# Optimization experiments

Hardware: AMD Instinct MI355X
Metric: run time of the kernel (lower is better)

## Reference

```python
import jax, jax.numpy as jnp
import numpy as np

B, T, C = 4, 4096, 512
H, KS = 8, 9
D = C // H
PAD = KS // 2


def setup_inputs() -> dict:
    key = jax.random.key(0)
    ks = jax.random.split(key, 9)
    s = 1.0 / np.sqrt(C)
    return {
        "x": jax.random.normal(ks[0], (B, T, C), jnp.float32),
        "Wq": jax.random.normal(ks[1], (C, C), jnp.float32) * s,
        "bq": jax.random.normal(ks[2], (C,), jnp.float32) * 0.01,
        "Wk": jax.random.normal(ks[3], (C, C), jnp.float32) * s,
        "bk": jax.random.normal(ks[4], (C,), jnp.float32) * 0.01,
        "Wv": jax.random.normal(ks[5], (C, C), jnp.float32) * s,
        "bv": jax.random.normal(ks[6], (C,), jnp.float32) * 0.01,
        "Wo": jax.random.normal(ks[7], (C, C), jnp.float32) * s,
        "bo": jax.random.normal(ks[8], (C,), jnp.float32) * 0.01,
    }


def reference(x, Wq, bq, Wk, bk, Wv, bv, Wo, bo):
    Bx, Tx, Cx = x.shape
    # projections (torch Linear: x @ W.T + b), split heads -> (B,H,T,D)
    q = (x @ Wq.T + bq).reshape(Bx, Tx, H, D).transpose(0, 2, 1, 3)
    k = (x @ Wk.T + bk).reshape(Bx, Tx, H, D).transpose(0, 2, 1, 3)
    v = (x @ Wv.T + bv).reshape(Bx, Tx, H, D).transpose(0, 2, 1, 3)
    # replicate-pad along time (matches F.pad mode='replicate')
    k_pad = jnp.pad(k, ((0, 0), (0, 0), (PAD, PAD), (0, 0)), mode='edge')
    v_pad = jnp.pad(v, ((0, 0), (0, 0), (PAD, PAD), (0, 0)), mode='edge')
    # window gather indices: (T, KS) into padded time axis
    idx = jnp.arange(Tx)[:, None] + jnp.arange(KS)[None, :]
    k_unf = k_pad[:, :, idx, :]  # (B,H,T,KS,D)
    v_unf = v_pad[:, :, idx, :]  # (B,H,T,KS,D)
    scale = 1.0 / np.sqrt(D)
    scores = jnp.einsum('bhtd,bhtkd->bhtk', q, k_unf) * scale  # (B,H,T,KS)
    attn = jax.nn.softmax(scores, axis=-1)
    y = jnp.einsum('bhtk,bhtkd->bhtd', attn, v_unf)  # (B,H,T,D)
    y = y.transpose(0, 2, 1, 3).reshape(Bx, Tx, Cx)
    return y @ Wo.T + bo
```

## Files before the change

kernel.cpp:

```cpp
#include <hip/hip_runtime.h>
#include <hip/hip_bf16.h>

#define B_    4
#define T_    4096
#define C_    512
#define H_    8
#define D_    64
#define KS_   9
#define PAD_  4
#define MTOT  (B_ * T_)
#define PLANE (MTOT * C_)
#define WU    (C_ * C_ / 8)

typedef __bf16 bf16_t;
typedef __bf16 bf16x8 __attribute__((ext_vector_type(8)));
typedef float  f32x4  __attribute__((ext_vector_type(4)));

__global__ __launch_bounds__(256)
void conv_all(const float* __restrict__ Wq, const float* __restrict__ Wk,
              const float* __restrict__ Wv, const float* __restrict__ Wo,
              const float* __restrict__ x,
              bf16_t* __restrict__ Wb, bf16_t* __restrict__ xb) {
  int i = blockIdx.x * 256 + threadIdx.x;
  const float* src;
  bf16_t* dst;
  if (i < 4 * WU) {
    int w = i >> 15;
    const float* W = (w == 0) ? Wq : (w == 1) ? Wk : (w == 2) ? Wv : Wo;
    src = W + (size_t)(i & (WU - 1)) * 8;
    dst = Wb + (size_t)i * 8;
  } else {
    size_t j = (size_t)(i - 4 * WU);
    src = x + j * 8;
    dst = xb + j * 8;
  }
  float4 f0 = ((const float4*)src)[0];
  float4 f1 = ((const float4*)src)[1];
  bf16x8 o;
  o[0] = (bf16_t)f0.x; o[1] = (bf16_t)f0.y; o[2] = (bf16_t)f0.z; o[3] = (bf16_t)f0.w;
  o[4] = (bf16_t)f1.x; o[5] = (bf16_t)f1.y; o[6] = (bf16_t)f1.z; o[7] = (bf16_t)f1.w;
  *(bf16x8*)dst = o;
}

#define BM   256
#define BN   128
#define BK   64
#define NKT  (C_ / BK)
#define ASL  (BM * BK)
#define BSL  (BN * BK)
#define SLOT (ASL + BSL)

#define GLD(srcp, off) __builtin_amdgcn_global_load_lds(                     \
    (const __attribute__((address_space(1))) unsigned int*)(srcp),           \
    (__attribute__((address_space(3))) unsigned int*)(&sm[off]), 16, 0, 0)

template<int MODE>
__global__ __launch_bounds__(512, 2)
void gemm8p(const bf16_t* __restrict__ A, const bf16_t* __restrict__ Bw,
            const float* __restrict__ b0, const float* __restrict__ b1,
            const float* __restrict__ b2, void* __restrict__ Outp) {
  __shared__ __align__(16) bf16_t sm[3 * SLOT];

  constexpr int GX  = (MODE == 0) ? (3 * C_ / BN) : (C_ / BN);
  constexpr int NWG = GX * (MTOT / BM);
  constexpr int CPX = NWG / 8;

  const int ord = blockIdx.y * GX + blockIdx.x;
  const int lg  = (ord & 7) * CPX + (ord >> 3);
  const int n0  = (lg % GX) * BN;
  const int m0  = (lg / GX) * BM;

  const int tid  = threadIdx.x;
  const int lane = tid & 63;
  const int wave = tid >> 6;
  const int wm   = wave >> 2;
  const int wn   = wave & 3;

  const bf16_t* aSrc[4];
  const bf16_t* bSrc[2];
#pragma unroll
  for (int s = 0; s < 4; ++s) {
    int u = s * 512 + tid, r = u >> 3, ch = u & 7;
    int cs = (ch ^ (r & 7)) << 3;
    if (MODE == 0) {
      aSrc[s] = A + (size_t)(m0 + r) * C_ + cs;
    } else {
      int bb = m0 >> 12, t0 = m0 & (T_ - 1);
      aSrc[s] = A + ((size_t)bb * H_ * T_ + t0 + r) * D_ + cs;
    }
  }
#pragma unroll
  for (int s = 0; s < 2; ++s) {
    int u = s * 512 + tid, r = u >> 3, ch = u & 7;
    int cs = (ch ^ (r & 7)) << 3;
    bSrc[s] = Bw + (size_t)(n0 + r) * C_ + cs;
  }
  constexpr size_t ASTEP = (MODE == 0) ? (size_t)BK : (size_t)T_ * D_;

#pragma unroll
  for (int s = 0; s < 4; ++s) GLD(aSrc[s], (s * 512 + tid) * 8);
#pragma unroll
  for (int s = 0; s < 2; ++s) GLD(bSrc[s], ASL + (s * 512 + tid) * 8);
#pragma unroll
  for (int s = 0; s < 4; ++s) GLD(aSrc[s] + ASTEP, SLOT + (s * 512 + tid) * 8);
#pragma unroll
  for (int s = 0; s < 2; ++s) GLD(bSrc[s] + BK, SLOT + ASL + (s * 512 + tid) * 8);
  asm volatile("s_waitcnt vmcnt(6)" ::: "memory");
  __builtin_amdgcn_s_barrier();

  f32x4 acc[8][2] = {};
  const int lr  = lane & 15;
  const int lq  = lane >> 4;
  const int co0 = ((0 + lq) ^ (lane & 7)) << 3;
  const int co1 = ((4 + lq) ^ (lane & 7)) << 3;

  int rsl = 0;
  for (int kt = 0; kt < NKT; ++kt) {
    const bf16_t* arow = &sm[rsl * SLOT + (wm * 128 + lr) * 64];
    const bf16_t* brow = &sm[rsl * SLOT + ASL + (wn * 32 + lr) * 64];
    const int  wof = ((rsl == 0) ? 2 : rsl - 1) * SLOT;
    const bool st  = (kt + 2 < NKT);
    const size_t ka = (size_t)(kt + 2) * ASTEP;
    const size_t kb = (size_t)(kt + 2) * BK;

    bf16x8 af[4][2], bfr[2][2];

#pragma unroll
    for (int i = 0; i < 4; ++i) {
      af[i][0] = *(const bf16x8*)(arow + i * 1024 + co0);
      af[i][1] = *(const bf16x8*)(arow + i * 1024 + co1);
    }
#pragma unroll
    for (int nf = 0; nf < 2; ++nf) {
      bfr[nf][0] = *(const bf16x8*)(brow + nf * 1024 + co0);
      bfr[nf][1] = *(const bf16x8*)(brow + nf * 1024 + co1);
    }
    if (st) {
      GLD(aSrc[0] + ka, wof + (0 * 512 + tid) * 8);
      GLD(aSrc[1] + ka, wof + (1 * 512 + tid) * 8);
    }
    __builtin_amdgcn_sched_barrier(0);
    __builtin_amdgcn_s_barrier();
    asm volatile("s_waitcnt lgkmcnt(0)" ::: "memory");
    __builtin_amdgcn_sched_barrier(0);
    __builtin_amdgcn_s_setprio(1);
#pragma unroll
    for (int i = 0; i < 4; ++i)
#pragma unroll
      for (int kk = 0; kk < 2; ++kk)
        acc[i][0] = __builtin_amdgcn_mfma_f32_16x16x32_bf16(
            af[i][kk], bfr[0][kk], acc[i][0], 0, 0, 0);
    __builtin_amdgcn_s_setprio(0);
    __builtin_amdgcn_sched_barrier(0);
    __builtin_amdgcn_s_barrier();

    if (st) {
      GLD(aSrc[2] + ka, wof + (2 * 512 + tid) * 8);
      GLD(aSrc[3] + ka, wof + (3 * 512 + tid) * 8);
    }
    __builtin_amdgcn_sched_barrier(0);
    __builtin_amdgcn_s_barrier();
    __builtin_amdgcn_s_setprio(1);
#pragma unroll
    for (int i = 0; i < 4; ++i)
#pragma unroll
      for (int kk = 0; kk < 2; ++kk)
        acc[i][1] = __builtin_amdgcn_mfma_f32_16x16x32_bf16(
            af[i][kk], bfr[1][kk], acc[i][1], 0, 0, 0);
    __builtin_amdgcn_s_setprio(0);
    __builtin_amdgcn_sched_barrier(0);
    __builtin_amdgcn_s_barrier();

#pragma unroll
    for (int i = 0; i < 4; ++i) {
      af[i][0] = *(const bf16x8*)(arow + 4096 + i * 1024 + co0);
      af[i][1] = *(const bf16x8*)(arow + 4096 + i * 1024 + co1);
    }
    if (st) {
      GLD(bSrc[0] + kb, wof + ASL + (0 * 512 + tid) * 8);
      GLD(bSrc[1] + kb, wof + ASL + (1 * 512 + tid) * 8);
    }
    __builtin_amdgcn_sched_barrier(0);
    __builtin_amdgcn_s_barrier();
    asm volatile("s_waitcnt lgkmcnt(0)" ::: "memory");
    __builtin_amdgcn_sched_barrier(0);
    __builtin_amdgcn_s_setprio(1);
#pragma unroll
    for (int i = 0; i < 4; ++i)
#pragma unroll
      for (int kk = 0; kk < 2; ++kk)
        acc[4 + i][0] = __builtin_amdgcn_mfma_f32_16x16x32_bf16(
            af[i][kk], bfr[0][kk], acc[4 + i][0], 0, 0, 0);
    __builtin_amdgcn_s_setprio(0);
    __builtin_amdgcn_sched_barrier(0);
    __builtin_amdgcn_s_barrier();

    __builtin_amdgcn_s_setprio(1);
#pragma unroll
    for (int i = 0; i < 4; ++i)
#pragma unroll
      for (int kk = 0; kk < 2; ++kk)
        acc[4 + i][1] = __builtin_amdgcn_mfma_f32_16x16x32_bf16(
            af[i][kk], bfr[1][kk], acc[4 + i][1], 0, 0, 0);
    __builtin_amdgcn_s_setprio(0);
    __builtin_amdgcn_sched_barrier(0);
    if (kt < NKT - 2)       asm volatile("s_waitcnt vmcnt(6)" ::: "memory");
    else if (kt == NKT - 2) asm volatile("s_waitcnt vmcnt(0)" ::: "memory");
    __builtin_amdgcn_s_barrier();
    rsl = (rsl == 2) ? 0 : rsl + 1;
  }

  const int rq = (lane >> 4) << 2;
  if constexpr (MODE == 0) {
    const int z  = n0 >> 9;
    const float* bias = (z == 0) ? b0 : (z == 1) ? b1 : b2;
    const int bb = m0 >> 12;
    const int t0 = m0 & (T_ - 1);
    bf16_t* plane = (bf16_t*)Outp + (size_t)z * PLANE;
#pragma unroll
    for (int nf = 0; nf < 2; ++nf) {
      const int cc  = (n0 & (C_ - 1)) + wn * 32 + nf * 16 + lr;
      const int hh  = cc >> 6, dd = cc & 63;
      const float bvv = bias[cc];
      bf16_t* hb = plane + ((size_t)(bb * H_ + hh) * T_) * D_ + dd;
#pragma unroll
      for (int f = 0; f < 8; ++f)
#pragma unroll
        for (int r = 0; r < 4; ++r) {
          const int t = t0 + wm * 128 + f * 16 + rq + r;
          hb[(size_t)t * D_] = (bf16_t)(acc[f][nf][r] + bvv);
        }
    }
  } else {
    float* outp = (float*)Outp;
#pragma unroll
    for (int nf = 0; nf < 2; ++nf) {
      const int n = n0 + wn * 32 + nf * 16 + lr;
      const float bvv = b0[n];
#pragma unroll
      for (int f = 0; f < 8; ++f)
#pragma unroll
        for (int r = 0; r < 4; ++r) {
          const int m = m0 + wm * 128 + f * 16 + rq + r;
          outp[(size_t)m * C_ + n] = acc[f][nf][r] + bvv;
        }
    }
  }
}

__global__ __launch_bounds__(256)
void attn_kernel(const bf16_t* __restrict__ qkv, bf16_t* __restrict__ y) {
  const int tid  = threadIdx.x;
  const int sub  = tid & 7;
  const int tl   = tid >> 3;
  const int t    = blockIdx.x * 32 + tl;
  const int h    = blockIdx.y;
  const int b    = blockIdx.z;

  const size_t pl = (size_t)(b * H_ + h) * T_ * D_;
  const bf16_t* q = qkv + pl;
  const bf16_t* k = qkv + (size_t)PLANE + pl;
  const bf16_t* v = qkv + (size_t)2 * PLANE + pl;
  const int c = sub * 8;

  int tj[KS_];
#pragma unroll
  for (int j = 0; j < KS_; ++j) {
    int tt = t - PAD_ + j;
    tj[j] = tt < 0 ? 0 : (tt >= T_ ? T_ - 1 : tt);
  }

  bf16x8 q8 = *(const bf16x8*)(q + (size_t)t * D_ + c);
  float qf[8];
#pragma unroll
  for (int e = 0; e < 8; ++e) qf[e] = (float)q8[e];

  float s[KS_];
#pragma unroll
  for (int j = 0; j < KS_; ++j) {
    bf16x8 k8 = *(const bf16x8*)(k + (size_t)tj[j] * D_ + c);
    float d0 = 0.f;
#pragma unroll
    for (int e = 0; e < 8; ++e) d0 += qf[e] * (float)k8[e];
    s[j] = d0;
  }

#pragma unroll
  for (int m = 1; m < 8; m <<= 1)
#pragma unroll
    for (int j = 0; j < KS_; ++j) s[j] += __shfl_xor(s[j], m, 8);

  float mx = s[0];
#pragma unroll
  for (int j = 1; j < KS_; ++j) mx = fmaxf(mx, s[j]);
  float w[KS_], sum = 0.f;
#pragma unroll
  for (int j = 0; j < KS_; ++j) {
    w[j] = __expf((s[j] - mx) * 0.125f);
    sum += w[j];
  }
  const float inv = 1.f / sum;
#pragma unroll
  for (int j = 0; j < KS_; ++j) w[j] *= inv;

  float o[8] = {0.f, 0.f, 0.f, 0.f, 0.f, 0.f, 0.f, 0.f};
#pragma unroll
  for (int j = 0; j < KS_; ++j) {
    bf16x8 v8 = *(const bf16x8*)(v + (size_t)tj[j] * D_ + c);
#pragma unroll
    for (int e = 0; e < 8; ++e) o[e] += w[j] * (float)v8[e];
  }
  bf16x8 o8;
#pragma unroll
  for (int e = 0; e < 8; ++e) o8[e] = (bf16_t)o[e];
  *(bf16x8*)(y + pl + (size_t)t * D_ + c) = o8;
}

extern "C" void kernel_launch(void* const* d_in, const int* in_sizes, int n_in,
                              void* d_out, int out_size, void* d_ws, size_t ws_size,
                              hipStream_t stream) {
  const float* x  = (const float*)d_in[0];
  const float* Wq = (const float*)d_in[1];
  const float* bq = (const float*)d_in[2];
  const float* Wk = (const float*)d_in[3];
  const float* bk = (const float*)d_in[4];
  const float* Wv = (const float*)d_in[5];
  const float* bv = (const float*)d_in[6];
  const float* Wo = (const float*)d_in[7];
  const float* bo = (const float*)d_in[8];
  float* out = (float*)d_out;

  bf16_t* Wb  = (bf16_t*)d_ws;
  bf16_t* xb  = Wb + (size_t)4 * C_ * C_;
  bf16_t* qkv = xb + (size_t)PLANE;
  bf16_t* y   = xb;

  conv_all<<<(4 * WU + PLANE / 8) / 256, 256, 0, stream>>>(Wq, Wk, Wv, Wo, x, Wb, xb);
  gemm8p<0><<<dim3(3 * C_ / BN, MTOT / BM), 512, 0, stream>>>(
      xb, Wb, bq, bk, bv, qkv);
  attn_kernel<<<dim3(T_ / 32, H_, B_), 256, 0, stream>>>(qkv, y);
  gemm8p<1><<<dim3(C_ / BN, MTOT / BM), 512, 0, stream>>>(
      y, Wb + (size_t)3 * C_ * C_, bo, nullptr, nullptr, out);
}
```

Baseline: 167.9 us.

## Fuse fp32-to-bf16 conversion of x into QKV GEMM A-tile loading

Removes the separate conversion pass over x; the QKV GEMM now loads fp32 x into registers, converts to bf16, and writes the A tile to LDS, pipelined one stage ahead. The weight conversion kernel is kept alone. This saves the write and reread of a bf16 copy of x, but each GEMM column tile now reads fp32 A (double the bytes) and uses register staging instead of direct global-to-LDS loads, increasing register pressure.

```diff
diff --git a/kernel.cpp b/kernel.cpp
--- a/kernel.cpp
+++ b/kernel.cpp
@@ -17,29 +17,19 @@
 typedef float  f32x4  __attribute__((ext_vector_type(4)));
 
 __global__ __launch_bounds__(256)
-void conv_all(const float* __restrict__ Wq, const float* __restrict__ Wk,
-              const float* __restrict__ Wv, const float* __restrict__ Wo,
-              const float* __restrict__ x,
-              bf16_t* __restrict__ Wb, bf16_t* __restrict__ xb) {
+void conv_w(const float* __restrict__ Wq, const float* __restrict__ Wk,
+            const float* __restrict__ Wv, const float* __restrict__ Wo,
+            bf16_t* __restrict__ dst) {
   int i = blockIdx.x * 256 + threadIdx.x;
-  const float* src;
-  bf16_t* dst;
-  if (i < 4 * WU) {
-    int w = i >> 15;
-    const float* W = (w == 0) ? Wq : (w == 1) ? Wk : (w == 2) ? Wv : Wo;
-    src = W + (size_t)(i & (WU - 1)) * 8;
-    dst = Wb + (size_t)i * 8;
-  } else {
-    size_t j = (size_t)(i - 4 * WU);
-    src = x + j * 8;
-    dst = xb + j * 8;
-  }
-  float4 f0 = ((const float4*)src)[0];
-  float4 f1 = ((const float4*)src)[1];
+  int w = i >> 15;
+  const float* W = (w == 0) ? Wq : (w == 1) ? Wk : (w == 2) ? Wv : Wo;
+  const float* s = W + (size_t)(i & (WU - 1)) * 8;
+  float4 f0 = ((const float4*)s)[0];
+  float4 f1 = ((const float4*)s)[1];
   bf16x8 o;
   o[0] = (bf16_t)f0.x; o[1] = (bf16_t)f0.y; o[2] = (bf16_t)f0.z; o[3] = (bf16_t)f0.w;
   o[4] = (bf16_t)f1.x; o[5] = (bf16_t)f1.y; o[6] = (bf16_t)f1.z; o[7] = (bf16_t)f1.w;
-  *(bf16x8*)dst = o;
+  ((bf16x8*)dst)[i] = o;
 }
 
 #define BM   256
@@ -56,7 +46,7 @@
 
 template<int MODE>
 __global__ __launch_bounds__(512, 2)
-void gemm8p(const bf16_t* __restrict__ A, const bf16_t* __restrict__ Bw,
+void gemm8p(const void* __restrict__ Ap, const bf16_t* __restrict__ Bw,
             const float* __restrict__ b0, const float* __restrict__ b1,
             const float* __restrict__ b2, void* __restrict__ Outp) {
   __shared__ __align__(16) bf16_t sm[3 * SLOT];
@@ -76,17 +66,18 @@
   const int wm   = wave >> 2;
   const int wn   = wave & 3;
 
-  const bf16_t* aSrc[4];
+  const float*  aF[4];
+  const bf16_t* aB[4];
   const bf16_t* bSrc[2];
 #pragma unroll
   for (int s = 0; s < 4; ++s) {
     int u = s * 512 + tid, r = u >> 3, ch = u & 7;
     int cs = (ch ^ (r & 7)) << 3;
-    if (MODE == 0) {
-      aSrc[s] = A + (size_t)(m0 + r) * C_ + cs;
+    if constexpr (MODE == 0) {
+      aF[s] = (const float*)Ap + (size_t)(m0 + r) * C_ + cs;
     } else {
       int bb = m0 >> 12, t0 = m0 & (T_ - 1);
-      aSrc[s] = A + ((size_t)bb * H_ * T_ + t0 + r) * D_ + cs;
+      aB[s] = (const bf16_t*)Ap + ((size_t)bb * H_ * T_ + t0 + r) * D_ + cs;
     }
   }
 #pragma unroll
@@ -95,17 +86,47 @@
     int cs = (ch ^ (r & 7)) << 3;
     bSrc[s] = Bw + (size_t)(n0 + r) * C_ + cs;
   }
-  constexpr size_t ASTEP = (MODE == 0) ? (size_t)BK : (size_t)T_ * D_;
-
-#pragma unroll
-  for (int s = 0; s < 4; ++s) GLD(aSrc[s], (s * 512 + tid) * 8);
-#pragma unroll
-  for (int s = 0; s < 2; ++s) GLD(bSrc[s], ASL + (s * 512 + tid) * 8);
-#pragma unroll
-  for (int s = 0; s < 4; ++s) GLD(aSrc[s] + ASTEP, SLOT + (s * 512 + tid) * 8);
-#pragma unroll
-  for (int s = 0; s < 2; ++s) GLD(bSrc[s] + BK, SLOT + ASL + (s * 512 + tid) * 8);
-  asm volatile("s_waitcnt vmcnt(6)" ::: "memory");
+
+  f32x4 areg[4][2];
+#define LDF4(p)   (((const f32x4*)(p))[0])
+#define WRA(s, off) do {                                                     \
+    bf16x8 wv_;                                                              \
+    wv_[0] = (bf16_t)areg[s][0][0]; wv_[1] = (bf16_t)areg[s][0][1];          \
+    wv_[2] = (bf16_t)areg[s][0][2]; wv_[3] = (bf16_t)areg[s][0][3];          \
+    wv_[4] = (bf16_t)areg[s][1][0]; wv_[5] = (bf16_t)areg[s][1][1];          \
+    wv_[6] = (bf16_t)areg[s][1][2]; wv_[7] = (bf16_t)areg[s][1][3];          \
+    *(bf16x8*)&sm[(off) + ((s) * 512 + tid) * 8] = wv_;                      \
+  } while (0)
+
+  if constexpr (MODE == 0) {
+#pragma unroll
+    for (int s = 0; s < 4; ++s) {
+      areg[s][0] = LDF4(aF[s]);     areg[s][1] = LDF4(aF[s] + 4);
+    }
+#pragma unroll
+    for (int s = 0; s < 4; ++s) WRA(s, 0);
+#pragma unroll
+    for (int s = 0; s < 2; ++s) GLD(bSrc[s], ASL + (s * 512 + tid) * 8);
+#pragma unroll
+    for (int s = 0; s < 4; ++s) {
+      areg[s][0] = LDF4(aF[s] + BK); areg[s][1] = LDF4(aF[s] + BK + 4);
+    }
+#pragma unroll
+    for (int s = 0; s < 2; ++s) GLD(bSrc[s] + BK, SLOT + ASL + (s * 512 + tid) * 8);
+    asm volatile("s_waitcnt vmcnt(10)" ::: "memory");
+  } else {
+    constexpr size_t AS = (size_t)T_ * D_;
+#pragma unroll
+    for (int s = 0; s < 4; ++s) GLD(aB[s], (s * 512 + tid) * 8);
+#pragma unroll
+    for (int s = 0; s < 2; ++s) GLD(bSrc[s], ASL + (s * 512 + tid) * 8);
+#pragma unroll
+    for (int s = 0; s < 4; ++s) GLD(aB[s] + AS, SLOT + (s * 512 + tid) * 8);
+#pragma unroll
+    for (int s = 0; s < 2; ++s) GLD(bSrc[s] + BK, SLOT + ASL + (s * 512 + tid) * 8);
+    asm volatile("s_waitcnt vmcnt(6)" ::: "memory");
+  }
+  asm volatile("s_waitcnt lgkmcnt(0)" ::: "memory");
   __builtin_amdgcn_s_barrier();
 
   f32x4 acc[8][2] = {};
@@ -118,10 +139,11 @@
   for (int kt = 0; kt < NKT; ++kt) {
     const bf16_t* arow = &sm[rsl * SLOT + (wm * 128 + lr) * 64];
     const bf16_t* brow = &sm[rsl * SLOT + ASL + (wn * 32 + lr) * 64];
-    const int  wof = ((rsl == 0) ? 2 : rsl - 1) * SLOT;
-    const bool st  = (kt + 2 < NKT);
-    const size_t ka = (size_t)(kt + 2) * ASTEP;
-    const size_t kb = (size_t)(kt + 2) * BK;
+    const int wA = ((rsl == 2) ? 0 : rsl + 1) * SLOT;
+    const int wB = ((rsl == 0) ? 2 : rsl - 1) * SLOT;
+    const bool w1 = (kt + 1 < NKT);
+    const bool st = (kt + 2 < NKT);
+    const size_t ka = (size_t)(kt + 2) * BK;
 
     bf16x8 af[4][2], bfr[2][2];
 
@@ -135,9 +157,18 @@
       bfr[nf][0] = *(const bf16x8*)(brow + nf * 1024 + co0);
       bfr[nf][1] = *(const bf16x8*)(brow + nf * 1024 + co1);
     }
-    if (st) {
-      GLD(aSrc[0] + ka, wof + (0 * 512 + tid) * 8);
-      GLD(aSrc[1] + ka, wof + (1 * 512 + tid) * 8);
+    if constexpr (MODE == 0) {
+      if (w1) { WRA(0, wA); WRA(1, wA); }
+      if (st) {
+        areg[0][0] = LDF4(aF[0] + ka); areg[0][1] = LDF4(aF[0] + ka + 4);
+        areg[1][0] = LDF4(aF[1] + ka); areg[1][1] = LDF4(aF[1] + ka + 4);
+      }
+    } else {
+      constexpr size_t AS = (size_t)T_ * D_;
+      if (st) {
+        GLD(aB[0] + (size_t)(kt + 2) * AS, wB + (0 * 512 + tid) * 8);
+        GLD(aB[1] + (size_t)(kt + 2) * AS, wB + (1 * 512 + tid) * 8);
+      }
     }
     __builtin_amdgcn_sched_barrier(0);
     __builtin_amdgcn_s_barrier();
@@ -154,9 +185,18 @@
     __builtin_amdgcn_sched_barrier(0);
     __builtin_amdgcn_s_barrier();
 
-    if (st) {
-      GLD(aSrc[2] + ka, wof + (2 * 512 + tid) * 8);
-      GLD(aSrc[3] + ka, wof + (3 * 512 + tid) * 8);
+    if constexpr (MODE == 0) {
+      if (w1) { WRA(2, wA); WRA(3, wA); }
+      if (st) {
+        areg[2][0] = LDF4(aF[2] + ka); areg[2][1] = LDF4(aF[2] + ka + 4);
+        areg[3][0] = LDF4(aF[3] + ka); areg[3][1] = LDF4(aF[3] + ka + 4);
+      }
+    } else {
+      constexpr size_t AS = (size_t)T_ * D_;
+      if (st) {
+        GLD(aB[2] + (size_t)(kt + 2) * AS, wB + (2 * 512 + tid) * 8);
+        GLD(aB[3] + (size_t)(kt + 2) * AS, wB + (3 * 512 + tid) * 8);
+      }
     }
     __builtin_amdgcn_sched_barrier(0);
     __builtin_amdgcn_s_barrier();
@@ -177,8 +217,8 @@
       af[i][1] = *(const bf16x8*)(arow + 4096 + i * 1024 + co1);
     }
     if (st) {
-      GLD(bSrc[0] + kb, wof + ASL + (0 * 512 + tid) * 8);
-      GLD(bSrc[1] + kb, wof + ASL + (1 * 512 + tid) * 8);
+      GLD(bSrc[0] + ka, wB + ASL + (0 * 512 + tid) * 8);
+      GLD(bSrc[1] + ka, wB + ASL + (1 * 512 + tid) * 8);
     }
     __builtin_amdgcn_sched_barrier(0);
     __builtin_amdgcn_s_barrier();
@@ -204,8 +244,13 @@
             af[i][kk], bfr[1][kk], acc[4 + i][1], 0, 0, 0);
     __builtin_amdgcn_s_setprio(0);
     __builtin_amdgcn_sched_barrier(0);
-    if (kt < NKT - 2)       asm volatile("s_waitcnt vmcnt(6)" ::: "memory");
-    else if (kt == NKT - 2) asm volatile("s_waitcnt vmcnt(0)" ::: "memory");
+    if constexpr (MODE == 0) {
+      if (kt < NKT - 2)       asm volatile("s_waitcnt vmcnt(10)" ::: "memory");
+      else if (kt == NKT - 2) asm volatile("s_waitcnt vmcnt(0)" ::: "memory");
+    } else {
+      if (kt < NKT - 2)       asm volatile("s_waitcnt vmcnt(6)" ::: "memory");
+      else if (kt == NKT - 2) asm volatile("s_waitcnt vmcnt(0)" ::: "memory");
+    }
     __builtin_amdgcn_s_barrier();
     rsl = (rsl == 2) ? 0 : rsl + 1;
   }
@@ -331,13 +376,12 @@
   float* out = (float*)d_out;
 
   bf16_t* Wb  = (bf16_t*)d_ws;
-  bf16_t* xb  = Wb + (size_t)4 * C_ * C_;
-  bf16_t* qkv = xb + (size_t)PLANE;
-  bf16_t* y   = xb;
-
-  conv_all<<<(4 * WU + PLANE / 8) / 256, 256, 0, stream>>>(Wq, Wk, Wv, Wo, x, Wb, xb);
+  bf16_t* qkv = Wb + (size_t)4 * C_ * C_;
+  bf16_t* y   = qkv + (size_t)3 * PLANE;
+
+  conv_w<<<4 * WU / 256, 256, 0, stream>>>(Wq, Wk, Wv, Wo, Wb);
   gemm8p<0><<<dim3(3 * C_ / BN, MTOT / BM), 512, 0, stream>>>(
-      xb, Wb, bq, bk, bv, qkv);
+      x, Wb, bq, bk, bv, qkv);
   attn_kernel<<<dim3(T_ / 32, H_, B_), 256, 0, stream>>>(qkv, y);
   gemm8p<1><<<dim3(C_ / BN, MTOT / BM), 512, 0, stream>>>(
       y, Wb + (size_t)3 * C_ * C_, bo, nullptr, nullptr, out);
```

Result: slower. 188.1 us (+12.1%).

## Rearrange GEMM wave tiling from 2x4 to 4x2 square 64x64 per wave

Applied to the files above, without the earlier changes.

Changes the per-wave tile in the projection GEMM from 128x32 (2x4 wave grid) to 64x64 (4x2 wave grid), so each wave loads 4 A fragments and 4 B fragments instead of 8 A and 2 B per k-step. The LDS reads are regrouped across the four MFMA phases, with an extra lgkmcnt wait before the second phase. This is meant to balance A/B fragment reuse and cut LDS read traffic per MFMA. The epilogue store pattern also changes, which may affect write coalescing.

```diff
diff --git a/kernel.cpp b/kernel.cpp
--- a/kernel.cpp
+++ b/kernel.cpp
@@ -73,8 +73,8 @@
   const int tid  = threadIdx.x;
   const int lane = tid & 63;
   const int wave = tid >> 6;
-  const int wm   = wave >> 2;
-  const int wn   = wave & 3;
+  const int wm   = wave >> 1;
+  const int wn   = wave & 1;
 
   const bf16_t* aSrc[4];
   const bf16_t* bSrc[2];
@@ -82,7 +82,7 @@
   for (int s = 0; s < 4; ++s) {
     int u = s * 512 + tid, r = u >> 3, ch = u & 7;
     int cs = (ch ^ (r & 7)) << 3;
-    if (MODE == 0) {
+    if constexpr (MODE == 0) {
       aSrc[s] = A + (size_t)(m0 + r) * C_ + cs;
     } else {
       int bb = m0 >> 12, t0 = m0 & (T_ - 1);
@@ -108,7 +108,7 @@
   asm volatile("s_waitcnt vmcnt(6)" ::: "memory");
   __builtin_amdgcn_s_barrier();
 
-  f32x4 acc[8][2] = {};
+  f32x4 acc[4][4] = {};
   const int lr  = lane & 15;
   const int lq  = lane >> 4;
   const int co0 = ((0 + lq) ^ (lane & 7)) << 3;
@@ -116,24 +116,21 @@
 
   int rsl = 0;
   for (int kt = 0; kt < NKT; ++kt) {
-    const bf16_t* arow = &sm[rsl * SLOT + (wm * 128 + lr) * 64];
-    const bf16_t* brow = &sm[rsl * SLOT + ASL + (wn * 32 + lr) * 64];
+    const bf16_t* arow = &sm[rsl * SLOT + (wm * 64 + lr) * 64];
+    const bf16_t* brow = &sm[rsl * SLOT + ASL + (wn * 64 + lr) * 64];
     const int  wof = ((rsl == 0) ? 2 : rsl - 1) * SLOT;
     const bool st  = (kt + 2 < NKT);
     const size_t ka = (size_t)(kt + 2) * ASTEP;
     const size_t kb = (size_t)(kt + 2) * BK;
 
-    bf16x8 af[4][2], bfr[2][2];
-
-#pragma unroll
-    for (int i = 0; i < 4; ++i) {
-      af[i][0] = *(const bf16x8*)(arow + i * 1024 + co0);
-      af[i][1] = *(const bf16x8*)(arow + i * 1024 + co1);
-    }
-#pragma unroll
-    for (int nf = 0; nf < 2; ++nf) {
-      bfr[nf][0] = *(const bf16x8*)(brow + nf * 1024 + co0);
-      bfr[nf][1] = *(const bf16x8*)(brow + nf * 1024 + co1);
+    bf16x8 af[4][2], bfr[4][2];
+
+#pragma unroll
+    for (int i = 0; i < 2; ++i) {
+      af[i][0]  = *(const bf16x8*)(arow + i * 1024 + co0);
+      af[i][1]  = *(const bf16x8*)(arow + i * 1024 + co1);
+      bfr[i][0] = *(const bf16x8*)(brow + i * 1024 + co0);
+      bfr[i][1] = *(const bf16x8*)(brow + i * 1024 + co1);
     }
     if (st) {
       GLD(aSrc[0] + ka, wof + (0 * 512 + tid) * 8);
@@ -145,36 +142,47 @@
     __builtin_amdgcn_sched_barrier(0);
     __builtin_amdgcn_s_setprio(1);
 #pragma unroll
-    for (int i = 0; i < 4; ++i)
-#pragma unroll
-      for (int kk = 0; kk < 2; ++kk)
-        acc[i][0] = __builtin_amdgcn_mfma_f32_16x16x32_bf16(
-            af[i][kk], bfr[0][kk], acc[i][0], 0, 0, 0);
+    for (int i = 0; i < 2; ++i)
+#pragma unroll
+      for (int j = 0; j < 2; ++j)
+#pragma unroll
+        for (int kk = 0; kk < 2; ++kk)
+          acc[i][j] = __builtin_amdgcn_mfma_f32_16x16x32_bf16(
+              af[i][kk], bfr[j][kk], acc[i][j], 0, 0, 0);
     __builtin_amdgcn_s_setprio(0);
     __builtin_amdgcn_sched_barrier(0);
     __builtin_amdgcn_s_barrier();
 
+#pragma unroll
+    for (int j = 2; j < 4; ++j) {
+      bfr[j][0] = *(const bf16x8*)(brow + j * 1024 + co0);
+      bfr[j][1] = *(const bf16x8*)(brow + j * 1024 + co1);
+    }
     if (st) {
       GLD(aSrc[2] + ka, wof + (2 * 512 + tid) * 8);
       GLD(aSrc[3] + ka, wof + (3 * 512 + tid) * 8);
     }
     __builtin_amdgcn_sched_barrier(0);
     __builtin_amdgcn_s_barrier();
+    asm volatile("s_waitcnt lgkmcnt(0)" ::: "memory");
+    __builtin_amdgcn_sched_barrier(0);
     __builtin_amdgcn_s_setprio(1);
 #pragma unroll
-    for (int i = 0; i < 4; ++i)
-#pragma unroll
-      for (int kk = 0; kk < 2; ++kk)
-        acc[i][1] = __builtin_amdgcn_mfma_f32_16x16x32_bf16(
-            af[i][kk], bfr[1][kk], acc[i][1], 0, 0, 0);
+    for (int i = 0; i < 2; ++i)
+#pragma unroll
+      for (int j = 2; j < 4; ++j)
+#pragma unroll
+        for (int kk = 0; kk < 2; ++kk)
+          acc[i][j] = __builtin_amdgcn_mfma_f32_16x16x32_bf16(
+              af[i][kk], bfr[j][kk], acc[i][j], 0, 0, 0);
     __builtin_amdgcn_s_setprio(0);
     __builtin_amdgcn_sched_barrier(0);
     __builtin_amdgcn_s_barrier();
 
 #pragma unroll
-    for (int i = 0; i < 4; ++i) {
-      af[i][0] = *(const bf16x8*)(arow + 4096 + i * 1024 + co0);
-      af[i][1] = *(const bf16x8*)(arow + 4096 + i * 1024 + co1);
+    for (int i = 2; i < 4; ++i) {
+      af[i][0] = *(const bf16x8*)(arow + i * 1024 + co0);
+      af[i][1] = *(const bf16x8*)(arow + i * 1024 + co1);
     }
     if (st) {
       GLD(bSrc[0] + kb, wof + ASL + (0 * 512 + tid) * 8);
@@ -186,22 +194,26 @@
     __builtin_amdgcn_sched_barrier(0);
     __builtin_amdgcn_s_setprio(1);
 #pragma unroll
-    for (int i = 0; i < 4; ++i)
-#pragma unroll
-      for (int kk = 0; kk < 2; ++kk)
-        acc[4 + i][0] = __builtin_amdgcn_mfma_f32_16x16x32_bf16(
-            af[i][kk], bfr[0][kk], acc[4 + i][0], 0, 0, 0);
+    for (int i = 2; i < 4; ++i)
+#pragma unroll
+      for (int j = 0; j < 2; ++j)
+#pragma unroll
+        for (int kk = 0; kk < 2; ++kk)
+          acc[i][j] = __builtin_amdgcn_mfma_f32_16x16x32_bf16(
+              af[i][kk], bfr[j][kk], acc[i][j], 0, 0, 0);
     __builtin_amdgcn_s_setprio(0);
     __builtin_amdgcn_sched_barrier(0);
     __builtin_amdgcn_s_barrier();
 
     __builtin_amdgcn_s_setprio(1);
 #pragma unroll
-    for (int i = 0; i < 4; ++i)
-#pragma unroll
-      for (int kk = 0; kk < 2; ++kk)
-        acc[4 + i][1] = __builtin_amdgcn_mfma_f32_16x16x32_bf16(
-            af[i][kk], bfr[1][kk], acc[4 + i][1], 0, 0, 0);
+    for (int i = 2; i < 4; ++i)
+#pragma unroll
+      for (int j = 2; j < 4; ++j)
+#pragma unroll
+        for (int kk = 0; kk < 2; ++kk)
+          acc[i][j] = __builtin_amdgcn_mfma_f32_16x16x32_bf16(
+              af[i][kk], bfr[j][kk], acc[i][j], 0, 0, 0);
     __builtin_amdgcn_s_setprio(0);
     __builtin_amdgcn_sched_barrier(0);
     if (kt < NKT - 2)       asm volatile("s_waitcnt vmcnt(6)" ::: "memory");
@@ -210,6 +222,7 @@
     rsl = (rsl == 2) ? 0 : rsl + 1;
   }
 
+  const int cn = lane & 15;
   const int rq = (lane >> 4) << 2;
   if constexpr (MODE == 0) {
     const int z  = n0 >> 9;
@@ -218,31 +231,31 @@
     const int t0 = m0 & (T_ - 1);
     bf16_t* plane = (bf16_t*)Outp + (size_t)z * PLANE;
 #pragma unroll
-    for (int nf = 0; nf < 2; ++nf) {
-      const int cc  = (n0 & (C_ - 1)) + wn * 32 + nf * 16 + lr;
+    for (int j = 0; j < 4; ++j) {
+      const int cc  = (n0 & (C_ - 1)) + wn * 64 + j * 16 + cn;
       const int hh  = cc >> 6, dd = cc & 63;
       const float bvv = bias[cc];
       bf16_t* hb = plane + ((size_t)(bb * H_ + hh) * T_) * D_ + dd;
 #pragma unroll
-      for (int f = 0; f < 8; ++f)
+      for (int i = 0; i < 4; ++i)
 #pragma unroll
         for (int r = 0; r < 4; ++r) {
-          const int t = t0 + wm * 128 + f * 16 + rq + r;
-          hb[(size_t)t * D_] = (bf16_t)(acc[f][nf][r] + bvv);
+          const int t = t0 + wm * 64 + i * 16 + rq + r;
+          hb[(size_t)t * D_] = (bf16_t)(acc[i][j][r] + bvv);
         }
     }
   } else {
     float* outp = (float*)Outp;
 #pragma unroll
-    for (int nf = 0; nf < 2; ++nf) {
-      const int n = n0 + wn * 32 + nf * 16 + lr;
+    for (int j = 0; j < 4; ++j) {
+      const int n = n0 + wn * 64 + j * 16 + cn;
       const float bvv = b0[n];
 #pragma unroll
-      for (int f = 0; f < 8; ++f)
+      for (int i = 0; i < 4; ++i)
 #pragma unroll
         for (int r = 0; r < 4; ++r) {
-          const int m = m0 + wm * 128 + f * 16 + rq + r;
-          outp[(size_t)m * C_ + n] = acc[f][nf][r] + bvv;
+          const int m = m0 + wm * 64 + i * 16 + rq + r;
+          outp[(size_t)m * C_ + n] = acc[i][j][r] + bvv;
         }
     }
   }
```

New measurement: 166.4 us. No clear change (-0.9%).
